# Optimization experiments

Hardware: AMD Instinct MI355X
Metric: run time of the kernel (lower is better)

Reference implementation:

```python
import jax, jax.numpy as jnp
import numpy as np

N, D, E, K = 8192, 4096, 64, 2

def setup_inputs() -> dict:
    key = jax.random.key(0)
    k1, k2 = jax.random.split(key)
    x = jax.random.normal(k1, (N, D), dtype=jnp.float32)
    W = jax.random.normal(k2, (E, D), dtype=jnp.float32) * (1.0 / np.sqrt(D))
    b = jnp.zeros((E,), dtype=jnp.float32)
    return {"x": x, "W": W, "b": b, "k": K}

def reference(x, W, b, k):
    # logits = x @ W^T + b : [N, E]
    logits = jnp.einsum('nd,ed->ne', x, W) + b
    probs = jax.nn.softmax(logits, axis=1)
    top_w, top_idx = jax.lax.top_k(probs, k)  # [N, k] each
    return (top_idx, top_w)
```

## Files before the change

kernel.cpp:

```cpp
#include <hip/hip_runtime.h>
#include <hip/hip_bf16.h>

#define N_ROWS 8192
#define D_DIM  4096
#define E_DIM  64
#define BR     16
#define BK     256
#define NCH    (D_DIM / BK)
#define NSTEP  (BK / 32)

typedef __attribute__((ext_vector_type(8))) short  short8;
typedef __attribute__((ext_vector_type(4))) float  floatx4;
typedef __attribute__((ext_vector_type(8))) float  float8;

__device__ inline void cvt_split(const float8& f, short8& hi, short8& lo) {
#pragma unroll
  for (int j = 0; j < 8; ++j) {
    float x = f[j];
    unsigned int u  = __builtin_bit_cast(unsigned int, x);
    unsigned int rh = (u + 0x7FFFu + ((u >> 16) & 1u)) >> 16;
    hi[j] = (short)rh;
    float hf = __builtin_bit_cast(float, rh << 16);
    float lf = x - hf;
    unsigned int ul = __builtin_bit_cast(unsigned int, lf);
    lo[j] = (short)(ul >> 16);
  }
}

__global__ __launch_bounds__(512) void prep_w(const void* __restrict__ xv,
                                              const void* __restrict__ wv,
                                              void* __restrict__ ws) {
  __shared__ int sflag;
  const int tid = threadIdx.x;
  if (tid < 64) {
    unsigned int v = ((const unsigned int*)xv)[(size_t)tid * 997];
    unsigned int e = (v >> 7) & 0xFFu;
    unsigned long long m = __ballot(e >= 100u && e <= 140u);
    if (tid == 0) sflag = (__popcll(m) > 32) ? 1 : 0;
  }
  __syncthreads();
  if (sflag) return;
  const int t    = blockIdx.x * 512 + tid;
  const int lane = t & 63;
  const int idx  = t >> 6;
  const int s    = idx >> 2;
  const int e    = idx & 3;
  const int row  = e * 16 + (lane & 15);
  const int col  = s * 32 + (lane >> 4) * 8;
  float8 f = *(const float8*)((const float*)wv + (size_t)row * D_DIM + col);
  short8 h, l;
  cvt_split(f, h, l);
  char* d = (char*)ws + (size_t)idx * 2048 + lane * 16;
  *(short8*)d          = h;
  *(short8*)(d + 1024) = l;
}

__global__ __launch_bounds__(256, 2) void router_kernel(
    const void* __restrict__ xv, const void* __restrict__ wv,
    const void* __restrict__ bv, const void* __restrict__ wsv,
    float* __restrict__ out) {
  __shared__ __align__(16) char sm[2][16384];
  __shared__ float lg[BR][E_DIM + 4];
  __shared__ int   sflag;

  const int tid = threadIdx.x;

  if (tid < 64) {
    unsigned int v = ((const unsigned int*)xv)[(size_t)tid * 997];
    unsigned int e = (v >> 7) & 0xFFu;
    unsigned long long m = __ballot(e >= 100u && e <= 140u);
    if (tid == 0) sflag = (__popcll(m) > 32) ? 1 : 0;
  }
  __syncthreads();
  const int isbf = sflag;

  const int wave = tid >> 6;
  const int lane = tid & 63;
  const int lm   = lane & 15;
  const int t4   = lane >> 4;
  const int r0   = blockIdx.x * BR;

  floatx4 acc = {0.f, 0.f, 0.f, 0.f};

  if (!isbf) {
    const int srow = tid >> 4;
    const int sc   = tid & 15;
    const float* xg = (const float*)xv + (size_t)(r0 + srow) * D_DIM + sc * 16;
    const int ws0 = srow * 512 + ((( sc * 2     ) ^ (srow & 7)) << 4);
    const int ws1 = srow * 512 + ((( sc * 2 + 1 ) ^ (srow & 7)) << 4);
    const char* wb = (const char*)wsv + (size_t)wave * 2048 + lane * 16;
    const int ra  = lm * 512;
    const int axr = lm & 7;

    short8 bh0, bh1, bh2, bh3, bh4, bh5, bh6, bh7;
    short8 bl0, bl1, bl2, bl3, bl4, bl5, bl6, bl7;

#define LDB(K, BASE)                                                       \
    bh##K = *(const short8*)((BASE) + (size_t)(K) * 8192);                 \
    bl##K = *(const short8*)((BASE) + (size_t)(K) * 8192 + 1024);

    LDB(0, wb) LDB(1, wb) LDB(2, wb) LDB(3, wb)
    LDB(4, wb) LDB(5, wb) LDB(6, wb) LDB(7, wb)
    {
      float8 f0 = *(const float8*)xg;
      float8 f1 = *(const float8*)(xg + 8);
      short8 h, l;
      char* d = sm[0];
      cvt_split(f0, h, l); *(short8*)(d + ws0) = h; *(short8*)(d + 8192 + ws0) = l;
      cvt_split(f1, h, l); *(short8*)(d + ws1) = h; *(short8*)(d + 8192 + ws1) = l;
    }
    __syncthreads();

    for (int i = 0; i < NCH; ++i) {
      float8 f0, f1;
      if (i + 1 < NCH) {
        const int o = (i + 1) * BK;
        f0 = *(const float8*)(xg + o);
        f1 = *(const float8*)(xg + o + 8);
      }
      const char* s   = sm[i & 1];
      const char* wbn = wb + (size_t)((i + 1 < NCH) ? i + 1 : i) * (NSTEP * 8192);

#define STEP(K)                                                            \
    {                                                                      \
      const int sa = ((((K) << 2) + t4) ^ axr) << 4;                       \
      short8 ah = *(const short8*)(s + ra + sa);                           \
      short8 al = *(const short8*)(s + ra + 8192 + sa);                    \
      acc = __builtin_amdgcn_mfma_f32_16x16x32_bf16(ah, bh##K, acc, 0, 0, 0); \
      acc = __builtin_amdgcn_mfma_f32_16x16x32_bf16(ah, bl##K, acc, 0, 0, 0); \
      acc = __builtin_amdgcn_mfma_f32_16x16x32_bf16(al, bh##K, acc, 0, 0, 0); \
      LDB(K, wbn)                                                          \
    }

      STEP(0) STEP(1) STEP(2) STEP(3)
      STEP(4) STEP(5) STEP(6) STEP(7)

      if (i + 1 < NCH) {
        char* d = sm[(i + 1) & 1];
        short8 h, l;
        cvt_split(f0, h, l); *(short8*)(d + ws0) = h; *(short8*)(d + 8192 + ws0) = l;
        cvt_split(f1, h, l); *(short8*)(d + ws1) = h; *(short8*)(d + 8192 + ws1) = l;
      }
      __syncthreads();
    }
#undef STEP
#undef LDB
  } else {
    const short* xp = (const short*)xv + (size_t)(r0 + lm) * D_DIM + t4 * 8;
    const short* wp = (const short*)wv + (size_t)(wave * 16 + lm) * D_DIM + t4 * 8;
    for (int k = 0; k < D_DIM; k += 64) {
      short8 a0 = *(const short8*)(xp + k);
      short8 b0 = *(const short8*)(wp + k);
      short8 a1 = *(const short8*)(xp + k + 32);
      short8 b1 = *(const short8*)(wp + k + 32);
      acc = __builtin_amdgcn_mfma_f32_16x16x32_bf16(a0, b0, acc, 0, 0, 0);
      acc = __builtin_amdgcn_mfma_f32_16x16x32_bf16(a1, b1, acc, 0, 0, 0);
    }
  }

  {
    const int col   = wave * 16 + lm;
    const int rbase = t4 << 2;
#pragma unroll
    for (int r = 0; r < 4; ++r) lg[rbase + r][col] = acc[r];
  }
  __syncthreads();

  if (tid < BR) {
    const int row = tid;
    float m1 = -3.4e38f, m2 = -3.4e38f;
    int   i1 = 0, i2 = 0;
    for (int e = 0; e < E_DIM; ++e) {
      float be = isbf ? __bfloat162float(((const __hip_bfloat16*)bv)[e])
                      : ((const float*)bv)[e];
      float l = lg[row][e] + be;
      if (l > m1)      { m2 = m1; i2 = i1; m1 = l; i1 = e; }
      else if (l > m2) { m2 = l;  i2 = e; }
    }
    float s = 0.f;
    for (int e = 0; e < E_DIM; ++e) {
      float be = isbf ? __bfloat162float(((const __hip_bfloat16*)bv)[e])
                      : ((const float*)bv)[e];
      s += expf(lg[row][e] + be - m1);
    }
    const int gr = r0 + row;
    out[2 * gr]                  = (float)i1;
    out[2 * gr + 1]              = (float)i2;
    out[2 * N_ROWS + 2 * gr]     = 1.0f / s;
    out[2 * N_ROWS + 2 * gr + 1] = expf(m2 - m1) / s;
  }
}

extern "C" void kernel_launch(void* const* d_in, const int* in_sizes, int n_in,
                              void* d_out, int out_size, void* d_ws, size_t ws_size,
                              hipStream_t stream) {
  (void)in_sizes; (void)n_in; (void)out_size; (void)ws_size;
  prep_w<<<dim3(64), dim3(512), 0, stream>>>(d_in[0], d_in[1], d_ws);
  router_kernel<<<dim3(N_ROWS / BR), dim3(256), 0, stream>>>(
      d_in[0], d_in[1], d_in[2], d_ws, (float*)d_out);
}
```

Baseline: 218.0 us.

## Stage fp32 x tiles into LDS via async global_load_lds, convert at consumer

The x tile is now copied straight from global memory into LDS as raw fp32 with global_load_lds, using an XOR-swizzled layout. This replaces the old path of loading into registers, splitting into bf16 hi/lo and writing to LDS. The hi/lo split now happens after the LDS read, inside each MFMA step. The aim is to make the x prefetch asynchronous and to free the registers used for staging. In exchange, every wave redoes the bf16 split for the shared A tile, so conversion ALU work grows roughly fourfold.

```diff
diff --git a/kernel.cpp b/kernel.cpp
--- a/kernel.cpp
+++ b/kernel.cpp
@@ -12,6 +12,12 @@
 typedef __attribute__((ext_vector_type(8))) short  short8;
 typedef __attribute__((ext_vector_type(4))) float  floatx4;
 typedef __attribute__((ext_vector_type(8))) float  float8;
+
+__device__ inline void gload16(const void* g, void* l) {
+  __builtin_amdgcn_global_load_lds(
+      (const __attribute__((address_space(1))) void*)g,
+      (__attribute__((address_space(3))) void*)l, 16, 0, 0);
+}
 
 __device__ inline void cvt_split(const float8& f, short8& hi, short8& lo) {
 #pragma unroll
@@ -59,7 +65,7 @@
     const void* __restrict__ xv, const void* __restrict__ wv,
     const void* __restrict__ bv, const void* __restrict__ wsv,
     float* __restrict__ out) {
-  __shared__ __align__(16) char sm[2][16384];
+  __shared__ __align__(16) char xs[2][16384];
   __shared__ float lg[BR][E_DIM + 4];
   __shared__ int   sflag;
 
@@ -83,13 +89,28 @@
   floatx4 acc = {0.f, 0.f, 0.f, 0.f};
 
   if (!isbf) {
-    const int srow = tid >> 4;
-    const int sc   = tid & 15;
-    const float* xg = (const float*)xv + (size_t)(r0 + srow) * D_DIM + sc * 16;
-    const int ws0 = srow * 512 + ((( sc * 2     ) ^ (srow & 7)) << 4);
-    const int ws1 = srow * 512 + ((( sc * 2 + 1 ) ^ (srow & 7)) << 4);
+    const char* xbase = (const char*)xv;
+    const char* g0 = xbase + (size_t)(r0 + 0*4 + wave) * (D_DIM * 4) +
+                     ((lane ^ ((0*4 + wave) & 7)) << 4);
+    const char* g1 = xbase + (size_t)(r0 + 1*4 + wave) * (D_DIM * 4) +
+                     ((lane ^ ((1*4 + wave) & 7)) << 4);
+    const char* g2 = xbase + (size_t)(r0 + 2*4 + wave) * (D_DIM * 4) +
+                     ((lane ^ ((2*4 + wave) & 7)) << 4);
+    const char* g3 = xbase + (size_t)(r0 + 3*4 + wave) * (D_DIM * 4) +
+                     ((lane ^ ((3*4 + wave) & 7)) << 4);
+    const int dof = wave << 10;
+
+#define STAGEX(BUF, CH)                                                    \
+    {                                                                      \
+      char* d = xs[BUF];                                                   \
+      gload16(g0 + (size_t)(CH) * 1024, d + 0 * 4096 + dof);               \
+      gload16(g1 + (size_t)(CH) * 1024, d + 1 * 4096 + dof);               \
+      gload16(g2 + (size_t)(CH) * 1024, d + 2 * 4096 + dof);               \
+      gload16(g3 + (size_t)(CH) * 1024, d + 3 * 4096 + dof);               \
+    }
+
     const char* wb = (const char*)wsv + (size_t)wave * 2048 + lane * 16;
-    const int ra  = lm * 512;
+    const int ra  = lm << 10;
     const int axr = lm & 7;
 
     short8 bh0, bh1, bh2, bh3, bh4, bh5, bh6, bh7;
@@ -101,31 +122,22 @@
 
     LDB(0, wb) LDB(1, wb) LDB(2, wb) LDB(3, wb)
     LDB(4, wb) LDB(5, wb) LDB(6, wb) LDB(7, wb)
-    {
-      float8 f0 = *(const float8*)xg;
-      float8 f1 = *(const float8*)(xg + 8);
-      short8 h, l;
-      char* d = sm[0];
-      cvt_split(f0, h, l); *(short8*)(d + ws0) = h; *(short8*)(d + 8192 + ws0) = l;
-      cvt_split(f1, h, l); *(short8*)(d + ws1) = h; *(short8*)(d + 8192 + ws1) = l;
-    }
+    STAGEX(0, 0)
     __syncthreads();
 
     for (int i = 0; i < NCH; ++i) {
-      float8 f0, f1;
-      if (i + 1 < NCH) {
-        const int o = (i + 1) * BK;
-        f0 = *(const float8*)(xg + o);
-        f1 = *(const float8*)(xg + o + 8);
-      }
-      const char* s   = sm[i & 1];
+      if (i + 1 < NCH) STAGEX((i + 1) & 1, i + 1);
+      const char* s   = xs[i & 1];
       const char* wbn = wb + (size_t)((i + 1 < NCH) ? i + 1 : i) * (NSTEP * 8192);
 
 #define STEP(K)                                                            \
     {                                                                      \
-      const int sa = ((((K) << 2) + t4) ^ axr) << 4;                       \
-      short8 ah = *(const short8*)(s + ra + sa);                           \
-      short8 al = *(const short8*)(s + ra + 8192 + sa);                    \
+      const int j2 = ((K) * 4 + t4) * 2;                                   \
+      floatx4 p0 = *(const floatx4*)(s + ra + ((j2 ^ axr) << 4));          \
+      floatx4 p1 = *(const floatx4*)(s + ra + (((j2 + 1) ^ axr) << 4));    \
+      float8 f = {p0[0], p0[1], p0[2], p0[3], p1[0], p1[1], p1[2], p1[3]}; \
+      short8 ah, al;                                                       \
+      cvt_split(f, ah, al);                                                \
       acc = __builtin_amdgcn_mfma_f32_16x16x32_bf16(ah, bh##K, acc, 0, 0, 0); \
       acc = __builtin_amdgcn_mfma_f32_16x16x32_bf16(ah, bl##K, acc, 0, 0, 0); \
       acc = __builtin_amdgcn_mfma_f32_16x16x32_bf16(al, bh##K, acc, 0, 0, 0); \
@@ -135,16 +147,11 @@
       STEP(0) STEP(1) STEP(2) STEP(3)
       STEP(4) STEP(5) STEP(6) STEP(7)
 
-      if (i + 1 < NCH) {
-        char* d = sm[(i + 1) & 1];
-        short8 h, l;
-        cvt_split(f0, h, l); *(short8*)(d + ws0) = h; *(short8*)(d + 8192 + ws0) = l;
-        cvt_split(f1, h, l); *(short8*)(d + ws1) = h; *(short8*)(d + 8192 + ws1) = l;
-      }
       __syncthreads();
     }
 #undef STEP
 #undef LDB
+#undef STAGEX
   } else {
     const short* xp = (const short*)xv + (size_t)(r0 + lm) * D_DIM + t4 * 8;
     const short* wp = (const short*)wv + (size_t)(wave * 16 + lm) * D_DIM + t4 * 8;
```

Result: no change. 219.3 us (+0.6%).
